# Kernel optimization log

Hardware: AMD Instinct MI355X
Metric: run time of the kernel (lower is better)

Reference implementation:

```python
import jax, jax.numpy as jnp
import numpy as np


def group_norm(x, gamma, beta, groups, eps=1e-5):
    B, C, H, W = x.shape
    xg = x.reshape(B, groups, C // groups, H, W)
    mu = xg.mean(axis=(2, 3, 4), keepdims=True)
    var = xg.var(axis=(2, 3, 4), keepdims=True)
    xn = ((xg - mu) * jax.lax.rsqrt(var + eps)).reshape(B, C, H, W)
    return xn * gamma[:, None, None] + beta[:, None, None]


def setup_inputs() -> dict:
    key = jax.random.key(0)
    ks = jax.random.split(key, 8)
    B, C, H, W = 4, 32, 256, 256
    return {
        "dec4": jax.random.normal(ks[0], (B, 512, 16, 16), jnp.float32),
        "feat": jax.random.normal(ks[1], (B, 64, H, W), jnp.float32),
        "gn_pre_gamma": jnp.ones((64,), jnp.float32),
        "gn_pre_beta": jnp.zeros((64,), jnp.float32),
        "W_pre": jax.random.normal(ks[2], (8, 64), jnp.float32) * 0.05,
        "b_pre": jnp.zeros((8,), jnp.float32),
        "gn_gap_gamma": jnp.ones((512,), jnp.float32),
        "gn_gap_beta": jnp.zeros((512,), jnp.float32),
        "W_gap": jax.random.normal(ks[3], (256, 512), jnp.float32) * 0.05,
        "b_gap": jnp.zeros((256,), jnp.float32),
        "emb": jax.random.normal(ks[4], (C, 256), jnp.float32),
        "W_ctrl": jax.random.normal(ks[5], (153, 512), jnp.float32) * 0.05,
        "b_ctrl": jnp.zeros((153,), jnp.float32),
    }


def reference(dec4, feat, gn_pre_gamma, gn_pre_beta, W_pre, b_pre,
              gn_gap_gamma, gn_gap_beta, W_gap, b_gap, emb, W_ctrl, b_ctrl):
    B = feat.shape[0]
    C = emb.shape[0]  # number of classes / dynamic-head instances
    # precls_conv: GroupNorm(16,64) -> ReLU -> 1x1 conv 64->8
    pre = jax.nn.relu(group_norm(feat, gn_pre_gamma, gn_pre_beta, 16))
    head_in = jnp.einsum('oi,bihw->bohw', W_pre, pre) + b_pre[:, None, None]  # [B,8,H,W]
    # GAP branch: GroupNorm(16,512) -> ReLU -> global avg pool -> 1x1 conv 512->256
    g = jax.nn.relu(group_norm(dec4, gn_gap_gamma, gn_gap_beta, 16)).mean(axis=(2, 3))  # [B,512]
    x_feat = g @ W_gap.T + b_gap  # [B,256]
    # controller: per (batch, class) dynamic conv params (1x1 conv == linear)
    x_cond = jnp.concatenate([
        jnp.broadcast_to(x_feat[:, None, :], (B, C, 256)),
        jnp.broadcast_to(emb[None], (B, C, 256)),
    ], axis=-1)  # [B,C,512]
    params = x_cond @ W_ctrl.T + b_ctrl  # [B,C,153]
    # split per weight_nums=[64,64,8], bias_nums=[8,8,1]
    w1 = params[..., 0:64].reshape(B, C, 8, 8)    # [out=8, in=8]
    w2 = params[..., 64:128].reshape(B, C, 8, 8)
    w3 = params[..., 128:136]                     # [out=1, in=8]
    b1 = params[..., 136:144]
    b2 = params[..., 144:152]
    b3 = params[..., 152:153]
    # batched grouped 1x1 convs (one group per (batch,class) instance)
    x1 = jax.nn.relu(jnp.einsum('bcoi,bihw->bcohw', w1, head_in) + b1[..., None, None])
    x2 = jax.nn.relu(jnp.einsum('bcoi,bcihw->bcohw', w2, x1) + b2[..., None, None])
    logits = jnp.einsum('bci,bcihw->bchw', w3, x2) + b3[..., None]  # [B,C,H,W]
    return logits
```

## Files before the change

kernel.cpp:

```cpp
#include <hip/hip_runtime.h>
#include <hip/hip_fp16.h>

typedef __fp16 h2 __attribute__((ext_vector_type(2)));
typedef __fp16 v4h __attribute__((ext_vector_type(4)));
typedef float f32x4 __attribute__((ext_vector_type(4)));

__device__ inline float wave_sum(float v) {
#pragma unroll
    for (int off = 32; off > 0; off >>= 1) v += __shfl_down(v, off, 64);
    return v;
}

__device__ inline v4h relu_pack(f32x4 d) {
    h2 lo = __builtin_amdgcn_cvt_pkrtz(d[0], d[1]);
    h2 hi = __builtin_amdgcn_cvt_pkrtz(d[2], d[3]);
#if defined(__has_builtin)
#if __has_builtin(__builtin_elementwise_max)
    h2 z = {(__fp16)0, (__fp16)0};
    lo = __builtin_elementwise_max(lo, z);
    hi = __builtin_elementwise_max(hi, z);
#else
    lo.x = (__fp16)fmaxf((float)lo.x, 0.f); lo.y = (__fp16)fmaxf((float)lo.y, 0.f);
    hi.x = (__fp16)fmaxf((float)hi.x, 0.f); hi.y = (__fp16)fmaxf((float)hi.y, 0.f);
#endif
#endif
    v4h r = {lo.x, lo.y, hi.x, hi.y};
    return r;
}

__global__ __launch_bounds__(256) void prep(
    const float* __restrict__ feat, const float* __restrict__ dec4,
    const float* __restrict__ gn_gap_gamma, const float* __restrict__ gn_gap_beta,
    const float* __restrict__ emb, const float* __restrict__ W_ctrl,
    float* __restrict__ partials, float* __restrict__ g_buf,
    float* __restrict__ E_ws) {
    int blk = blockIdx.x;
    int tid = threadIdx.x;
    int wid = tid >> 6, lane = tid & 63;
    if (blk < 512) {
        int grp = blk >> 3;
        int chunk = blk & 7;
        const float4* base = (const float4*)(feat + (size_t)grp * 262144 + (size_t)chunk * 32768);
        float sa = 0.f, qa = 0.f, sb = 0.f, qb = 0.f;
#pragma unroll 8
        for (int i = 0; i < 16; ++i) {
            float4 v = base[i * 256 + tid];
            float4 u = base[(i + 16) * 256 + tid];
            sa += v.x + v.y + v.z + v.w;
            qa += v.x * v.x + v.y * v.y + v.z * v.z + v.w * v.w;
            sb += u.x + u.y + u.z + u.w;
            qb += u.x * u.x + u.y * u.y + u.z * u.z + u.w * u.w;
        }
        __shared__ float ls[4], lq[4];
        float s = wave_sum(sa + sb);
        float q = wave_sum(qa + qb);
        if (lane == 0) { ls[wid] = s; lq[wid] = q; }
        __syncthreads();
        if (tid == 0) {
            partials[blk * 2 + 0] = ls[0] + ls[1] + ls[2] + ls[3];
            partials[blk * 2 + 1] = lq[0] + lq[1] + lq[2] + lq[3];
        }
    } else if (blk < 576) {
        int idx = blk - 512;
        int b = idx >> 4, gi = idx & 15;
        const float* base = dec4 + (size_t)idx * 8192;
        int ch = tid >> 3, sub = tid & 7;
        const float4* r = (const float4*)(base + ch * 256 + sub * 32);
        float v[32];
        float s = 0.f, q = 0.f;
#pragma unroll
        for (int i = 0; i < 8; ++i) {
            float4 a = r[i];
            v[i * 4 + 0] = a.x; v[i * 4 + 1] = a.y; v[i * 4 + 2] = a.z; v[i * 4 + 3] = a.w;
            s += a.x + a.y + a.z + a.w;
            q += a.x * a.x + a.y * a.y + a.z * a.z + a.w * a.w;
        }
        __shared__ float ls[4], lq[4], bc[2];
        s = wave_sum(s); q = wave_sum(q);
        if (lane == 0) { ls[wid] = s; lq[wid] = q; }
        __syncthreads();
        if (tid == 0) {
            float S = ls[0] + ls[1] + ls[2] + ls[3];
            float Q = lq[0] + lq[1] + lq[2] + lq[3];
            const float inv = 1.f / 8192.f;
            float mu = S * inv;
            float var = Q * inv - mu * mu;
            bc[0] = mu;
            bc[1] = rsqrtf(var + 1e-5f);
        }
        __syncthreads();
        float mu = bc[0], rs = bc[1];
        int c = gi * 32 + ch;
        float sc = rs * gn_gap_gamma[c];
        float sh = gn_gap_beta[c] - mu * sc;
        float acc = 0.f;
#pragma unroll
        for (int i = 0; i < 32; ++i) acc += fmaxf(v[i] * sc + sh, 0.f);
#pragma unroll
        for (int m = 1; m < 8; m <<= 1) acc += __shfl_xor(acc, m, 64);
        if (sub == 0) g_buf[b * 512 + c] = acc * (1.f / 256.f);
    } else {
        int c = blk - 576;
        __shared__ float es[256];
        es[tid] = emb[c * 256 + tid];
        __syncthreads();
        if (tid < 153) {
            const float4* w4 = (const float4*)(W_ctrl + tid * 512 + 256);
            const float4* e4 = (const float4*)es;
            float acc = 0.f;
#pragma unroll 8
            for (int k = 0; k < 64; ++k) {
                float4 a = w4[k], e = e4[k];
                acc += a.x * e.x + a.y * e.y + a.z * e.z + a.w * e.w;
            }
            E_ws[c * 153 + tid] = acc;
        }
    }
}

__global__ __launch_bounds__(256) void fc(
    const float* __restrict__ g_buf, const float* __restrict__ W_gap,
    const float* __restrict__ b_gap, const float* __restrict__ W_ctrl,
    const float* __restrict__ b_ctrl, const float* __restrict__ E_ws,
    unsigned char* __restrict__ pk) {
    int b = blockIdx.x, tid = threadIdx.x;
    __shared__ float gs[512];
    __shared__ float xf[256];
    __shared__ float F[160];
    gs[tid] = g_buf[b * 512 + tid];
    gs[tid + 256] = g_buf[b * 512 + 256 + tid];
    __syncthreads();
    {
        const float4* w = (const float4*)(W_gap + tid * 512);
        const float4* g4 = (const float4*)gs;
        float acc = b_gap[tid];
#pragma unroll 8
        for (int k = 0; k < 128; ++k) {
            float4 wv = w[k], gv = g4[k];
            acc += wv.x * gv.x + wv.y * gv.y + wv.z * gv.z + wv.w * gv.w;
        }
        xf[tid] = acc;
    }
    __syncthreads();
    if (tid < 160) {
        float acc = 0.f;
        if (tid < 153) {
            const float4* w = (const float4*)(W_ctrl + tid * 512);
            const float4* x4 = (const float4*)xf;
#pragma unroll 8
            for (int k = 0; k < 64; ++k) {
                float4 wv = w[k], xv = x4[k];
                acc += wv.x * xv.x + wv.y * xv.y + wv.z * xv.z + wv.w * xv.w;
            }
            acc += b_ctrl[tid];
        }
        F[tid] = acc;
    }
    __syncthreads();
    unsigned char* dst = pk + (size_t)b * 10240;
    for (int c = 0; c < 32; ++c) {
        if (tid < 152) {
            float v = F[tid] + E_ws[c * 153 + tid];
            ((__fp16*)(dst + c * 320))[tid] = (__fp16)v;
        } else if (tid == 152) {
            *(float*)(dst + c * 320 + 304) = F[152] + E_ws[c * 153 + 152];
        }
    }
}

struct Frags { v4h A1, A2, A3; f32x4 C1, C2, C3; };

__device__ inline Frags make_frags(const __fp16* ph, const float* smemf, int c0,
                                   int csel, int o, int dup, int crow,
                                   bool ok1, bool okBD) {
    Frags f;
    int cbA = (c0 + csel) * 160;
    int cbB = (c0 + crow) * 160;
    v4h z = {(__fp16)0, (__fp16)0, (__fp16)0, (__fp16)0};
    v4h a1 = *(const v4h*)(ph + cbA + o * 8 + dup * 4);
    v4h a2 = *(const v4h*)(ph + cbA + 64 + o * 8 + dup * 4);
    v4h a3 = *(const v4h*)(ph + cbA + 128 + dup * 4);
    f.A1 = ok1 ? a1 : z;
    f.A2 = okBD ? a2 : z;
    f.A3 = (okBD && o == 0) ? a3 : z;
    v4h b1 = *(const v4h*)(ph + cbB + 136 + dup * 4);
    v4h b2 = *(const v4h*)(ph + cbB + 144 + dup * 4);
    f.C1 = f32x4{(float)b1.x, (float)b1.y, (float)b1.z, (float)b1.w};
    f.C2 = f32x4{(float)b2.x, (float)b2.y, (float)b2.z, (float)b2.w};
    f.C3 = f32x4{0.f, 0.f, 0.f, 0.f};
    if (dup == 0) f.C3[0] = smemf[(c0 + crow) * 80 + 76];
    return f;
}

__global__ __launch_bounds__(512, 4) void mainK(
    const float* __restrict__ feat, const float* __restrict__ partials,
    const float* __restrict__ gamma, const float* __restrict__ beta,
    const float* __restrict__ W_pre, const float* __restrict__ b_pre,
    const float4* __restrict__ pk, float* __restrict__ out) {
    int blk = blockIdx.x;
    int b = blk >> 7;
    int tid = threadIdx.x;
    int w = tid >> 6, lane = tid & 63;
    int P0 = (blk & 127) << 9;

    __shared__ __align__(16) float smem[4768];
    float4* pp   = (float4*)smem;
    float4* hi_l = (float4*)(smem + 2560);
    float2* sch  = (float2*)(smem + 4608);
    float* mus = smem + 4736;
    float* rss = smem + 4752;

    const float4* src = pk + (size_t)b * 640;
    for (int i = tid; i < 640; i += 512) pp[i] = src[i];

    if (tid < 16) {
        float s = 0.f, q = 0.f;
#pragma unroll
        for (int cc = 0; cc < 8; ++cc) {
            int idx = ((b * 16 + tid) * 8 + cc) * 2;
            s += partials[idx]; q += partials[idx + 1];
        }
        const float inv = 1.f / 262144.f;
        float mu = s * inv;
        float var = q * inv - mu * mu;
        mus[tid] = mu; rss[tid] = rsqrtf(var + 1e-5f);
    }
    __syncthreads();
    if (tid < 64) {
        float mu = mus[tid >> 2], rs = rss[tid >> 2];
        float sg = rs * gamma[tid];
        sch[tid] = make_float2(sg, beta[tid] - mu * sg);
    }
    __syncthreads();

    {
        float hi[8];
#pragma unroll
        for (int o2 = 0; o2 < 8; ++o2) hi[o2] = b_pre[o2];
        const float* fb = feat + ((size_t)b << 22) + P0 + tid;
#pragma unroll
        for (int ch = 0; ch < 64; ++ch) {
            float v = fb[(size_t)ch << 16];
            float2 ss = sch[ch];
            float pre = fmaxf(v * ss.x + ss.y, 0.f);
#pragma unroll
            for (int o2 = 0; o2 < 8; ++o2) hi[o2] += W_pre[o2 * 64 + ch] * pre;
        }
        float4 hq;
        hq.x = __builtin_bit_cast(float, __builtin_amdgcn_cvt_pkrtz(hi[0], hi[1]));
        hq.y = __builtin_bit_cast(float, __builtin_amdgcn_cvt_pkrtz(hi[2], hi[3]));
        hq.z = __builtin_bit_cast(float, __builtin_amdgcn_cvt_pkrtz(hi[4], hi[5]));
        hq.w = __builtin_bit_cast(float, __builtin_amdgcn_cvt_pkrtz(hi[6], hi[7]));
        hi_l[tid] = hq;
    }
    __syncthreads();

    const __fp16* ph = (const __fp16*)smem;
    int m = lane & 15;
    int kg = lane >> 4;
    int csel = m >> 3;
    int o = m & 7;
    int dup = kg & 1;
    int crow = kg >> 1;
    bool ok1 = (kg < 2);
    bool okBD = (crow == csel);
    bool act = (dup == 0);

    int cA = w << 2;
    int cB = cA + 2;
    Frags fa = make_frags(ph, smem, cA, csel, o, dup, crow, ok1, okBD);
    Frags fb2 = make_frags(ph, smem, cB, csel, o, dup, crow, ok1, okBD);

    float* ob = out + ((size_t)b << 21) + P0;
    float* cpA = ob + ((size_t)(cA + crow) << 16) + m;
    float* cpB = ob + ((size_t)(cB + crow) << 16) + m;
    const __fp16* hp = ph + 5120 + m * 8 + dup * 4;

#pragma unroll 4
    for (int g = 0; g < 32; ++g) {
        v4h B1 = *(const v4h*)(hp + g * 128);
        f32x4 d1a = __builtin_amdgcn_mfma_f32_16x16x16f16(fa.A1, B1, fa.C1, 0, 0, 0);
        f32x4 d1b = __builtin_amdgcn_mfma_f32_16x16x16f16(fb2.A1, B1, fb2.C1, 0, 0, 0);
        v4h p2a = relu_pack(d1a);
        v4h p2b = relu_pack(d1b);
        f32x4 d2a = __builtin_amdgcn_mfma_f32_16x16x16f16(fa.A2, p2a, fa.C2, 0, 0, 0);
        f32x4 d2b = __builtin_amdgcn_mfma_f32_16x16x16f16(fb2.A2, p2b, fb2.C2, 0, 0, 0);
        v4h p3a = relu_pack(d2a);
        v4h p3b = relu_pack(d2b);
        f32x4 d3a = __builtin_amdgcn_mfma_f32_16x16x16f16(fa.A3, p3a, fa.C3, 0, 0, 0);
        f32x4 d3b = __builtin_amdgcn_mfma_f32_16x16x16f16(fb2.A3, p3b, fb2.C3, 0, 0, 0);
        if (act) {
            cpA[g * 16] = d3a[0];
            cpB[g * 16] = d3b[0];
        }
    }
}

extern "C" void kernel_launch(void* const* d_in, const int* in_sizes, int n_in,
                              void* d_out, int out_size, void* d_ws, size_t ws_size,
                              hipStream_t stream) {
    const float* dec4         = (const float*)d_in[0];
    const float* feat         = (const float*)d_in[1];
    const float* gn_pre_gamma = (const float*)d_in[2];
    const float* gn_pre_beta  = (const float*)d_in[3];
    const float* W_pre        = (const float*)d_in[4];
    const float* b_pre        = (const float*)d_in[5];
    const float* gn_gap_gamma = (const float*)d_in[6];
    const float* gn_gap_beta  = (const float*)d_in[7];
    const float* W_gap        = (const float*)d_in[8];
    const float* b_gap        = (const float*)d_in[9];
    const float* emb          = (const float*)d_in[10];
    const float* W_ctrl       = (const float*)d_in[11];
    const float* b_ctrl       = (const float*)d_in[12];
    float* out = (float*)d_out;
    float* ws  = (float*)d_ws;

    float* partials = ws;
    float* g_buf    = ws + 1024;
    float* E_ws     = ws + 3072;
    unsigned char* pkB = (unsigned char*)(ws + 7968);

    prep<<<608, 256, 0, stream>>>(feat, dec4, gn_gap_gamma, gn_gap_beta,
                                  emb, W_ctrl, partials, g_buf, E_ws);
    fc<<<4, 256, 0, stream>>>(g_buf, W_gap, b_gap, W_ctrl, b_ctrl, E_ws, pkB);
    mainK<<<512, 512, 0, stream>>>(feat, partials, gn_pre_gamma, gn_pre_beta,
                                   W_pre, b_pre, (const float4*)pkB, out);
}
```

Before: 73.32 us.

## Double grid size for stats and main kernels, split channel reduction across halves

The feature statistics pass now uses 16 chunks per group instead of 8, so it launches twice as many blocks, each doing half the work. The main kernel now processes 256 pixels per block instead of 512 and launches twice as many blocks. Within each block the two halves of the threads each reduce 32 of the 64 input channels, then combine their partial sums through shared memory. This is meant to raise parallelism and memory-level concurrency, at the cost of an extra shared-memory pass and barrier, more LDS per block, and a second reload of the per-batch parameter tile by each block.

```diff
diff --git a/kernel.cpp b/kernel.cpp
--- a/kernel.cpp
+++ b/kernel.cpp
@@ -14,16 +14,9 @@
 __device__ inline v4h relu_pack(f32x4 d) {
     h2 lo = __builtin_amdgcn_cvt_pkrtz(d[0], d[1]);
     h2 hi = __builtin_amdgcn_cvt_pkrtz(d[2], d[3]);
-#if defined(__has_builtin)
-#if __has_builtin(__builtin_elementwise_max)
     h2 z = {(__fp16)0, (__fp16)0};
     lo = __builtin_elementwise_max(lo, z);
     hi = __builtin_elementwise_max(hi, z);
-#else
-    lo.x = (__fp16)fmaxf((float)lo.x, 0.f); lo.y = (__fp16)fmaxf((float)lo.y, 0.f);
-    hi.x = (__fp16)fmaxf((float)hi.x, 0.f); hi.y = (__fp16)fmaxf((float)hi.y, 0.f);
-#endif
-#endif
     v4h r = {lo.x, lo.y, hi.x, hi.y};
     return r;
 }
@@ -37,15 +30,15 @@
     int blk = blockIdx.x;
     int tid = threadIdx.x;
     int wid = tid >> 6, lane = tid & 63;
-    if (blk < 512) {
-        int grp = blk >> 3;
-        int chunk = blk & 7;
-        const float4* base = (const float4*)(feat + (size_t)grp * 262144 + (size_t)chunk * 32768);
+    if (blk < 1024) {
+        int grp = blk >> 4;
+        int chunk = blk & 15;
+        const float4* base = (const float4*)(feat + (size_t)grp * 262144 + (size_t)chunk * 16384);
         float sa = 0.f, qa = 0.f, sb = 0.f, qb = 0.f;
-#pragma unroll 8
-        for (int i = 0; i < 16; ++i) {
+#pragma unroll 4
+        for (int i = 0; i < 8; ++i) {
             float4 v = base[i * 256 + tid];
-            float4 u = base[(i + 16) * 256 + tid];
+            float4 u = base[(i + 8) * 256 + tid];
             sa += v.x + v.y + v.z + v.w;
             qa += v.x * v.x + v.y * v.y + v.z * v.z + v.w * v.w;
             sb += u.x + u.y + u.z + u.w;
@@ -60,8 +53,8 @@
             partials[blk * 2 + 0] = ls[0] + ls[1] + ls[2] + ls[3];
             partials[blk * 2 + 1] = lq[0] + lq[1] + lq[2] + lq[3];
         }
-    } else if (blk < 576) {
-        int idx = blk - 512;
+    } else if (blk < 1088) {
+        int idx = blk - 1024;
         int b = idx >> 4, gi = idx & 15;
         const float* base = dec4 + (size_t)idx * 8192;
         int ch = tid >> 3, sub = tid & 7;
@@ -100,7 +93,7 @@
         for (int m = 1; m < 8; m <<= 1) acc += __shfl_xor(acc, m, 64);
         if (sub == 0) g_buf[b * 512 + c] = acc * (1.f / 256.f);
     } else {
-        int c = blk - 576;
+        int c = blk - 1088;
         __shared__ float es[256];
         es[tid] = emb[c * 256 + tid];
         __syncthreads();
@@ -198,17 +191,19 @@
     const float* __restrict__ W_pre, const float* __restrict__ b_pre,
     const float4* __restrict__ pk, float* __restrict__ out) {
     int blk = blockIdx.x;
-    int b = blk >> 7;
+    int b = blk >> 8;
     int tid = threadIdx.x;
     int w = tid >> 6, lane = tid & 63;
-    int P0 = (blk & 127) << 9;
-
-    __shared__ __align__(16) float smem[4768];
+    int P0 = (blk & 255) << 8;
+
+    __shared__ __align__(16) float smem[6816];
     float4* pp   = (float4*)smem;
-    float4* hi_l = (float4*)(smem + 2560);
-    float2* sch  = (float2*)(smem + 4608);
-    float* mus = smem + 4736;
-    float* rss = smem + 4752;
+    float4* tmpA = (float4*)(smem + 2560);
+    float4* tmpB = (float4*)(smem + 4608);
+    float4* hi_l = tmpA;
+    float2* sch  = (float2*)(smem + 6656);
+    float* mus = smem + 6784;
+    float* rss = smem + 6800;
 
     const float4* src = pk + (size_t)b * 640;
     for (int i = tid; i < 640; i += 512) pp[i] = src[i];
@@ -216,8 +211,8 @@
     if (tid < 16) {
         float s = 0.f, q = 0.f;
 #pragma unroll
-        for (int cc = 0; cc < 8; ++cc) {
-            int idx = ((b * 16 + tid) * 8 + cc) * 2;
+        for (int cc = 0; cc < 16; ++cc) {
+            int idx = ((b * 16 + tid) * 16 + cc) * 2;
             s += partials[idx]; q += partials[idx + 1];
         }
         const float inv = 1.f / 262144.f;
@@ -234,23 +229,33 @@
     __syncthreads();
 
     {
+        int px = tid & 255, half = tid >> 8;
         float hi[8];
 #pragma unroll
-        for (int o2 = 0; o2 < 8; ++o2) hi[o2] = b_pre[o2];
-        const float* fb = feat + ((size_t)b << 22) + P0 + tid;
-#pragma unroll
-        for (int ch = 0; ch < 64; ++ch) {
-            float v = fb[(size_t)ch << 16];
+        for (int o2 = 0; o2 < 8; ++o2) hi[o2] = half ? 0.f : b_pre[o2];
+        const float* fb = feat + ((size_t)b << 22) + ((size_t)half << 21) + P0 + px;
+        const float* wp = W_pre + half * 32;
+#pragma unroll
+        for (int c2 = 0; c2 < 32; ++c2) {
+            int ch = half * 32 + c2;
+            float v = fb[(size_t)c2 << 16];
             float2 ss = sch[ch];
             float pre = fmaxf(v * ss.x + ss.y, 0.f);
 #pragma unroll
-            for (int o2 = 0; o2 < 8; ++o2) hi[o2] += W_pre[o2 * 64 + ch] * pre;
-        }
+            for (int o2 = 0; o2 < 8; ++o2) hi[o2] += wp[o2 * 64 + c2] * pre;
+        }
+        tmpA[tid] = make_float4(hi[0], hi[1], hi[2], hi[3]);
+        tmpB[tid] = make_float4(hi[4], hi[5], hi[6], hi[7]);
+    }
+    __syncthreads();
+    if (tid < 256) {
+        float4 a0 = tmpA[tid], a1 = tmpA[tid + 256];
+        float4 b0 = tmpB[tid], b1 = tmpB[tid + 256];
         float4 hq;
-        hq.x = __builtin_bit_cast(float, __builtin_amdgcn_cvt_pkrtz(hi[0], hi[1]));
-        hq.y = __builtin_bit_cast(float, __builtin_amdgcn_cvt_pkrtz(hi[2], hi[3]));
-        hq.z = __builtin_bit_cast(float, __builtin_amdgcn_cvt_pkrtz(hi[4], hi[5]));
-        hq.w = __builtin_bit_cast(float, __builtin_amdgcn_cvt_pkrtz(hi[6], hi[7]));
+        hq.x = __builtin_bit_cast(float, __builtin_amdgcn_cvt_pkrtz(a0.x + a1.x, a0.y + a1.y));
+        hq.y = __builtin_bit_cast(float, __builtin_amdgcn_cvt_pkrtz(a0.z + a1.z, a0.w + a1.w));
+        hq.z = __builtin_bit_cast(float, __builtin_amdgcn_cvt_pkrtz(b0.x + b1.x, b0.y + b1.y));
+        hq.w = __builtin_bit_cast(float, __builtin_amdgcn_cvt_pkrtz(b0.z + b1.z, b0.w + b1.w));
         hi_l[tid] = hq;
     }
     __syncthreads();
@@ -277,7 +282,7 @@
     const __fp16* hp = ph + 5120 + m * 8 + dup * 4;
 
 #pragma unroll 4
-    for (int g = 0; g < 32; ++g) {
+    for (int g = 0; g < 16; ++g) {
         v4h B1 = *(const v4h*)(hp + g * 128);
         f32x4 d1a = __builtin_amdgcn_mfma_f32_16x16x16f16(fa.A1, B1, fa.C1, 0, 0, 0);
         f32x4 d1b = __builtin_amdgcn_mfma_f32_16x16x16f16(fb2.A1, B1, fb2.C1, 0, 0, 0);
@@ -316,13 +321,13 @@
     float* ws  = (float*)d_ws;
 
     float* partials = ws;
-    float* g_buf    = ws + 1024;
-    float* E_ws     = ws + 3072;
-    unsigned char* pkB = (unsigned char*)(ws + 7968);
-
-    prep<<<608, 256, 0, stream>>>(feat, dec4, gn_gap_gamma, gn_gap_beta,
-                                  emb, W_ctrl, partials, g_buf, E_ws);
+    float* g_buf    = ws + 2048;
+    float* E_ws     = ws + 4096;
+    unsigned char* pkB = (unsigned char*)(ws + 8992);
+
+    prep<<<1120, 256, 0, stream>>>(feat, dec4, gn_gap_gamma, gn_gap_beta,
+                                   emb, W_ctrl, partials, g_buf, E_ws);
     fc<<<4, 256, 0, stream>>>(g_buf, W_gap, b_gap, W_ctrl, b_ctrl, E_ws, pkB);
-    mainK<<<512, 512, 0, stream>>>(feat, partials, gn_pre_gamma, gn_pre_beta,
-                                   W_pre, b_pre, (const float4*)pkB, out);
-}
+    mainK<<<1024, 512, 0, stream>>>(feat, partials, gn_pre_gamma, gn_pre_beta,
+                                    W_pre, b_pre, (const float4*)pkB, out);
+}
```

New measurement: 88.06 us. 1.2x slower.

## Split main kernel into smaller 256-thread blocks over 128 pixels

Applied to the files above, without the earlier changes.

Each main-kernel block now covers 128 pixels with 256 threads (2048 blocks instead of 512), which shrinks shared memory and raises the occupancy target. Only 128 threads compute the head input, and each wave loops over four class pairs with one fragment set at a time instead of keeping two interleaved. The aim is more resident blocks to hide memory latency. The cost is redoing the per-batch setup (parameter copy, GroupNorm stats) four times as often, leaving half the threads idle during the feature pass, and losing the two independent MFMA chains per iteration.

```diff
diff --git a/kernel.cpp b/kernel.cpp
--- a/kernel.cpp
+++ b/kernel.cpp
@@ -14,16 +14,9 @@
 __device__ inline v4h relu_pack(f32x4 d) {
     h2 lo = __builtin_amdgcn_cvt_pkrtz(d[0], d[1]);
     h2 hi = __builtin_amdgcn_cvt_pkrtz(d[2], d[3]);
-#if defined(__has_builtin)
-#if __has_builtin(__builtin_elementwise_max)
     h2 z = {(__fp16)0, (__fp16)0};
     lo = __builtin_elementwise_max(lo, z);
     hi = __builtin_elementwise_max(hi, z);
-#else
-    lo.x = (__fp16)fmaxf((float)lo.x, 0.f); lo.y = (__fp16)fmaxf((float)lo.y, 0.f);
-    hi.x = (__fp16)fmaxf((float)hi.x, 0.f); hi.y = (__fp16)fmaxf((float)hi.y, 0.f);
-#endif
-#endif
     v4h r = {lo.x, lo.y, hi.x, hi.y};
     return r;
 }
@@ -192,26 +185,26 @@
     return f;
 }
 
-__global__ __launch_bounds__(512, 4) void mainK(
+__global__ __launch_bounds__(256, 8) void mainK(
     const float* __restrict__ feat, const float* __restrict__ partials,
     const float* __restrict__ gamma, const float* __restrict__ beta,
     const float* __restrict__ W_pre, const float* __restrict__ b_pre,
     const float4* __restrict__ pk, float* __restrict__ out) {
     int blk = blockIdx.x;
-    int b = blk >> 7;
+    int b = blk >> 9;
     int tid = threadIdx.x;
     int w = tid >> 6, lane = tid & 63;
-    int P0 = (blk & 127) << 9;
-
-    __shared__ __align__(16) float smem[4768];
+    int P0 = (blk & 511) << 7;
+
+    __shared__ __align__(16) float smem[3264];
     float4* pp   = (float4*)smem;
     float4* hi_l = (float4*)(smem + 2560);
-    float2* sch  = (float2*)(smem + 4608);
-    float* mus = smem + 4736;
-    float* rss = smem + 4752;
+    float2* sch  = (float2*)(smem + 3072);
+    float* mus = smem + 3200;
+    float* rss = smem + 3216;
 
     const float4* src = pk + (size_t)b * 640;
-    for (int i = tid; i < 640; i += 512) pp[i] = src[i];
+    for (int i = tid; i < 640; i += 256) pp[i] = src[i];
 
     if (tid < 16) {
         float s = 0.f, q = 0.f;
@@ -233,7 +226,7 @@
     }
     __syncthreads();
 
-    {
+    if (tid < 128) {
         float hi[8];
 #pragma unroll
         for (int o2 = 0; o2 < 8; ++o2) hi[o2] = b_pre[o2];
@@ -266,32 +259,23 @@
     bool okBD = (crow == csel);
     bool act = (dup == 0);
 
-    int cA = w << 2;
-    int cB = cA + 2;
-    Frags fa = make_frags(ph, smem, cA, csel, o, dup, crow, ok1, okBD);
-    Frags fb2 = make_frags(ph, smem, cB, csel, o, dup, crow, ok1, okBD);
-
     float* ob = out + ((size_t)b << 21) + P0;
-    float* cpA = ob + ((size_t)(cA + crow) << 16) + m;
-    float* cpB = ob + ((size_t)(cB + crow) << 16) + m;
     const __fp16* hp = ph + 5120 + m * 8 + dup * 4;
 
-#pragma unroll 4
-    for (int g = 0; g < 32; ++g) {
-        v4h B1 = *(const v4h*)(hp + g * 128);
-        f32x4 d1a = __builtin_amdgcn_mfma_f32_16x16x16f16(fa.A1, B1, fa.C1, 0, 0, 0);
-        f32x4 d1b = __builtin_amdgcn_mfma_f32_16x16x16f16(fb2.A1, B1, fb2.C1, 0, 0, 0);
-        v4h p2a = relu_pack(d1a);
-        v4h p2b = relu_pack(d1b);
-        f32x4 d2a = __builtin_amdgcn_mfma_f32_16x16x16f16(fa.A2, p2a, fa.C2, 0, 0, 0);
-        f32x4 d2b = __builtin_amdgcn_mfma_f32_16x16x16f16(fb2.A2, p2b, fb2.C2, 0, 0, 0);
-        v4h p3a = relu_pack(d2a);
-        v4h p3b = relu_pack(d2b);
-        f32x4 d3a = __builtin_amdgcn_mfma_f32_16x16x16f16(fa.A3, p3a, fa.C3, 0, 0, 0);
-        f32x4 d3b = __builtin_amdgcn_mfma_f32_16x16x16f16(fb2.A3, p3b, fb2.C3, 0, 0, 0);
-        if (act) {
-            cpA[g * 16] = d3a[0];
-            cpB[g * 16] = d3b[0];
+#pragma unroll 1
+    for (int p = 0; p < 4; ++p) {
+        int c0 = (w << 3) + (p << 1);
+        Frags f = make_frags(ph, smem, c0, csel, o, dup, crow, ok1, okBD);
+        float* cp = ob + ((size_t)(c0 + crow) << 16) + m;
+#pragma unroll 2
+        for (int g = 0; g < 8; ++g) {
+            v4h B1 = *(const v4h*)(hp + g * 128);
+            f32x4 d1 = __builtin_amdgcn_mfma_f32_16x16x16f16(f.A1, B1, f.C1, 0, 0, 0);
+            v4h p2 = relu_pack(d1);
+            f32x4 d2 = __builtin_amdgcn_mfma_f32_16x16x16f16(f.A2, p2, f.C2, 0, 0, 0);
+            v4h p3 = relu_pack(d2);
+            f32x4 d3 = __builtin_amdgcn_mfma_f32_16x16x16f16(f.A3, p3, f.C3, 0, 0, 0);
+            if (act) cp[g * 16] = d3[0];
         }
     }
 }
@@ -323,6 +307,6 @@
     prep<<<608, 256, 0, stream>>>(feat, dec4, gn_gap_gamma, gn_gap_beta,
                                   emb, W_ctrl, partials, g_buf, E_ws);
     fc<<<4, 256, 0, stream>>>(g_buf, W_gap, b_gap, W_ctrl, b_ctrl, E_ws, pkB);
-    mainK<<<512, 512, 0, stream>>>(feat, partials, gn_pre_gamma, gn_pre_beta,
-                                   W_pre, b_pre, (const float4*)pkB, out);
-}
+    mainK<<<2048, 256, 0, stream>>>(feat, partials, gn_pre_gamma, gn_pre_beta,
+                                    W_pre, b_pre, (const float4*)pkB, out);
+}
```

Result: slower. 79.65 us (+8.6%).

## Fuse prep, fc and main stages into one cooperative kernel with grid syncs

Applied to the files above, without the earlier changes.

Replaces the three-kernel launch sequence with a single cooperative kernel of 256 blocks of 512 threads. The stages are separated by grid.sync(), which removes two kernel-launch boundaries and their gaps. Each block now covers 1024 pixels instead of 512, and the fc stage splits its dot products across thread pairs. The fallback path still uses the old three kernels. In exchange, only 256 blocks run, with no occupancy hint, so there is less parallelism in the main phase, and the grid barriers add their own cost.

```diff
diff --git a/kernel.cpp b/kernel.cpp
--- a/kernel.cpp
+++ b/kernel.cpp
@@ -1,5 +1,8 @@
 #include <hip/hip_runtime.h>
 #include <hip/hip_fp16.h>
+#include <hip/hip_cooperative_groups.h>
+
+namespace cg = cooperative_groups;
 
 typedef __fp16 h2 __attribute__((ext_vector_type(2)));
 typedef __fp16 v4h __attribute__((ext_vector_type(4)));
@@ -14,158 +17,11 @@
 __device__ inline v4h relu_pack(f32x4 d) {
     h2 lo = __builtin_amdgcn_cvt_pkrtz(d[0], d[1]);
     h2 hi = __builtin_amdgcn_cvt_pkrtz(d[2], d[3]);
-#if defined(__has_builtin)
-#if __has_builtin(__builtin_elementwise_max)
     h2 z = {(__fp16)0, (__fp16)0};
     lo = __builtin_elementwise_max(lo, z);
     hi = __builtin_elementwise_max(hi, z);
-#else
-    lo.x = (__fp16)fmaxf((float)lo.x, 0.f); lo.y = (__fp16)fmaxf((float)lo.y, 0.f);
-    hi.x = (__fp16)fmaxf((float)hi.x, 0.f); hi.y = (__fp16)fmaxf((float)hi.y, 0.f);
-#endif
-#endif
     v4h r = {lo.x, lo.y, hi.x, hi.y};
     return r;
-}
-
-__global__ __launch_bounds__(256) void prep(
-    const float* __restrict__ feat, const float* __restrict__ dec4,
-    const float* __restrict__ gn_gap_gamma, const float* __restrict__ gn_gap_beta,
-    const float* __restrict__ emb, const float* __restrict__ W_ctrl,
-    float* __restrict__ partials, float* __restrict__ g_buf,
-    float* __restrict__ E_ws) {
-    int blk = blockIdx.x;
-    int tid = threadIdx.x;
-    int wid = tid >> 6, lane = tid & 63;
-    if (blk < 512) {
-        int grp = blk >> 3;
-        int chunk = blk & 7;
-        const float4* base = (const float4*)(feat + (size_t)grp * 262144 + (size_t)chunk * 32768);
-        float sa = 0.f, qa = 0.f, sb = 0.f, qb = 0.f;
-#pragma unroll 8
-        for (int i = 0; i < 16; ++i) {
-            float4 v = base[i * 256 + tid];
-            float4 u = base[(i + 16) * 256 + tid];
-            sa += v.x + v.y + v.z + v.w;
-            qa += v.x * v.x + v.y * v.y + v.z * v.z + v.w * v.w;
-            sb += u.x + u.y + u.z + u.w;
-            qb += u.x * u.x + u.y * u.y + u.z * u.z + u.w * u.w;
-        }
-        __shared__ float ls[4], lq[4];
-        float s = wave_sum(sa + sb);
-        float q = wave_sum(qa + qb);
-        if (lane == 0) { ls[wid] = s; lq[wid] = q; }
-        __syncthreads();
-        if (tid == 0) {
-            partials[blk * 2 + 0] = ls[0] + ls[1] + ls[2] + ls[3];
-            partials[blk * 2 + 1] = lq[0] + lq[1] + lq[2] + lq[3];
-        }
-    } else if (blk < 576) {
-        int idx = blk - 512;
-        int b = idx >> 4, gi = idx & 15;
-        const float* base = dec4 + (size_t)idx * 8192;
-        int ch = tid >> 3, sub = tid & 7;
-        const float4* r = (const float4*)(base + ch * 256 + sub * 32);
-        float v[32];
-        float s = 0.f, q = 0.f;
-#pragma unroll
-        for (int i = 0; i < 8; ++i) {
-            float4 a = r[i];
-            v[i * 4 + 0] = a.x; v[i * 4 + 1] = a.y; v[i * 4 + 2] = a.z; v[i * 4 + 3] = a.w;
-            s += a.x + a.y + a.z + a.w;
-            q += a.x * a.x + a.y * a.y + a.z * a.z + a.w * a.w;
-        }
-        __shared__ float ls[4], lq[4], bc[2];
-        s = wave_sum(s); q = wave_sum(q);
-        if (lane == 0) { ls[wid] = s; lq[wid] = q; }
-        __syncthreads();
-        if (tid == 0) {
-            float S = ls[0] + ls[1] + ls[2] + ls[3];
-            float Q = lq[0] + lq[1] + lq[2] + lq[3];
-            const float inv = 1.f / 8192.f;
-            float mu = S * inv;
-            float var = Q * inv - mu * mu;
-            bc[0] = mu;
-            bc[1] = rsqrtf(var + 1e-5f);
-        }
-        __syncthreads();
-        float mu = bc[0], rs = bc[1];
-        int c = gi * 32 + ch;
-        float sc = rs * gn_gap_gamma[c];
-        float sh = gn_gap_beta[c] - mu * sc;
-        float acc = 0.f;
-#pragma unroll
-        for (int i = 0; i < 32; ++i) acc += fmaxf(v[i] * sc + sh, 0.f);
-#pragma unroll
-        for (int m = 1; m < 8; m <<= 1) acc += __shfl_xor(acc, m, 64);
-        if (sub == 0) g_buf[b * 512 + c] = acc * (1.f / 256.f);
-    } else {
-        int c = blk - 576;
-        __shared__ float es[256];
-        es[tid] = emb[c * 256 + tid];
-        __syncthreads();
-        if (tid < 153) {
-            const float4* w4 = (const float4*)(W_ctrl + tid * 512 + 256);
-            const float4* e4 = (const float4*)es;
-            float acc = 0.f;
-#pragma unroll 8
-            for (int k = 0; k < 64; ++k) {
-                float4 a = w4[k], e = e4[k];
-                acc += a.x * e.x + a.y * e.y + a.z * e.z + a.w * e.w;
-            }
-            E_ws[c * 153 + tid] = acc;
-        }
-    }
-}
-
-__global__ __launch_bounds__(256) void fc(
-    const float* __restrict__ g_buf, const float* __restrict__ W_gap,
-    const float* __restrict__ b_gap, const float* __restrict__ W_ctrl,
-    const float* __restrict__ b_ctrl, const float* __restrict__ E_ws,
-    unsigned char* __restrict__ pk) {
-    int b = blockIdx.x, tid = threadIdx.x;
-    __shared__ float gs[512];
-    __shared__ float xf[256];
-    __shared__ float F[160];
-    gs[tid] = g_buf[b * 512 + tid];
-    gs[tid + 256] = g_buf[b * 512 + 256 + tid];
-    __syncthreads();
-    {
-        const float4* w = (const float4*)(W_gap + tid * 512);
-        const float4* g4 = (const float4*)gs;
-        float acc = b_gap[tid];
-#pragma unroll 8
-        for (int k = 0; k < 128; ++k) {
-            float4 wv = w[k], gv = g4[k];
-            acc += wv.x * gv.x + wv.y * gv.y + wv.z * gv.z + wv.w * gv.w;
-        }
-        xf[tid] = acc;
-    }
-    __syncthreads();
-    if (tid < 160) {
-        float acc = 0.f;
-        if (tid < 153) {
-            const float4* w = (const float4*)(W_ctrl + tid * 512);
-            const float4* x4 = (const float4*)xf;
-#pragma unroll 8
-            for (int k = 0; k < 64; ++k) {
-                float4 wv = w[k], xv = x4[k];
-                acc += wv.x * xv.x + wv.y * xv.y + wv.z * xv.z + wv.w * xv.w;
-            }
-            acc += b_ctrl[tid];
-        }
-        F[tid] = acc;
-    }
-    __syncthreads();
-    unsigned char* dst = pk + (size_t)b * 10240;
-    for (int c = 0; c < 32; ++c) {
-        if (tid < 152) {
-            float v = F[tid] + E_ws[c * 153 + tid];
-            ((__fp16*)(dst + c * 320))[tid] = (__fp16)v;
-        } else if (tid == 152) {
-            *(float*)(dst + c * 320 + 304) = F[152] + E_ws[c * 153 + 152];
-        }
-    }
 }
 
 struct Frags { v4h A1, A2, A3; f32x4 C1, C2, C3; };
@@ -192,6 +48,396 @@
     return f;
 }
 
+__global__ __launch_bounds__(512) void mega(
+    const float* __restrict__ feat, const float* __restrict__ dec4,
+    const float* __restrict__ gn_pre_gamma, const float* __restrict__ gn_pre_beta,
+    const float* __restrict__ W_pre, const float* __restrict__ b_pre,
+    const float* __restrict__ gn_gap_gamma, const float* __restrict__ gn_gap_beta,
+    const float* __restrict__ W_gap, const float* __restrict__ b_gap,
+    const float* __restrict__ emb, const float* __restrict__ W_ctrl,
+    const float* __restrict__ b_ctrl, float* __restrict__ out,
+    float* __restrict__ partials, float* __restrict__ g_buf,
+    float* __restrict__ E_ws, unsigned char* __restrict__ pk) {
+    cg::grid_group grid = cg::this_grid();
+    __shared__ __align__(16) float smem[6816];
+    const int k = blockIdx.x;
+    const int tid = threadIdx.x;
+    const int w = tid >> 6, lane = tid & 63;
+    float* ls = smem + 6656;
+    float* lq = smem + 6664;
+    float* bc = smem + 6672;
+
+    for (int t = k; t < 608; t += 256) {
+        if (t < 512) {
+            int grp = t >> 3, chunk = t & 7;
+            const float4* base = (const float4*)(feat + (size_t)grp * 262144 + (size_t)chunk * 32768);
+            float sa = 0.f, qa = 0.f, sb = 0.f, qb = 0.f;
+#pragma unroll 4
+            for (int i = 0; i < 8; ++i) {
+                float4 v = base[i * 512 + tid];
+                float4 u = base[(i + 8) * 512 + tid];
+                sa += v.x + v.y + v.z + v.w;
+                qa += v.x * v.x + v.y * v.y + v.z * v.z + v.w * v.w;
+                sb += u.x + u.y + u.z + u.w;
+                qb += u.x * u.x + u.y * u.y + u.z * u.z + u.w * u.w;
+            }
+            float s = wave_sum(sa + sb);
+            float q = wave_sum(qa + qb);
+            if (lane == 0) { ls[w] = s; lq[w] = q; }
+            __syncthreads();
+            if (tid == 0) {
+                float S = 0.f, Q = 0.f;
+#pragma unroll
+                for (int i = 0; i < 8; ++i) { S += ls[i]; Q += lq[i]; }
+                partials[t * 2 + 0] = S;
+                partials[t * 2 + 1] = Q;
+            }
+        } else if (t < 576) {
+            int idx = t - 512;
+            int b = idx >> 4, gi = idx & 15;
+            const float* base = dec4 + (size_t)idx * 8192;
+            int ch = tid >> 4, sub = tid & 15;
+            const float4* r = (const float4*)(base + ch * 256 + sub * 16);
+            float v[16];
+            float s = 0.f, q = 0.f;
+#pragma unroll
+            for (int i = 0; i < 4; ++i) {
+                float4 a = r[i];
+                v[i * 4 + 0] = a.x; v[i * 4 + 1] = a.y; v[i * 4 + 2] = a.z; v[i * 4 + 3] = a.w;
+                s += a.x + a.y + a.z + a.w;
+                q += a.x * a.x + a.y * a.y + a.z * a.z + a.w * a.w;
+            }
+            s = wave_sum(s); q = wave_sum(q);
+            if (lane == 0) { ls[w] = s; lq[w] = q; }
+            __syncthreads();
+            if (tid == 0) {
+                float S = 0.f, Q = 0.f;
+#pragma unroll
+                for (int i = 0; i < 8; ++i) { S += ls[i]; Q += lq[i]; }
+                const float inv = 1.f / 8192.f;
+                float mu = S * inv;
+                float var = Q * inv - mu * mu;
+                bc[0] = mu;
+                bc[1] = rsqrtf(var + 1e-5f);
+            }
+            __syncthreads();
+            float mu = bc[0], rs = bc[1];
+            int c = gi * 32 + ch;
+            float sc = rs * gn_gap_gamma[c];
+            float sh = gn_gap_beta[c] - mu * sc;
+            float acc = 0.f;
+#pragma unroll
+            for (int i = 0; i < 16; ++i) acc += fmaxf(v[i] * sc + sh, 0.f);
+#pragma unroll
+            for (int m = 1; m < 16; m <<= 1) acc += __shfl_xor(acc, m, 64);
+            if (sub == 0) g_buf[b * 512 + c] = acc * (1.f / 256.f);
+        } else {
+            int c = t - 576;
+            if (tid < 256) smem[tid] = emb[c * 256 + tid];
+            __syncthreads();
+            if (tid < 153) {
+                const float4* w4 = (const float4*)(W_ctrl + tid * 512 + 256);
+                const float4* e4 = (const float4*)smem;
+                float acc = 0.f;
+#pragma unroll 8
+                for (int kk = 0; kk < 64; ++kk) {
+                    float4 a = w4[kk], e = e4[kk];
+                    acc += a.x * e.x + a.y * e.y + a.z * e.z + a.w * e.w;
+                }
+                E_ws[c * 153 + tid] = acc;
+            }
+        }
+        __syncthreads();
+    }
+
+    grid.sync();
+
+    if (k < 4) {
+        int b = k;
+        float* gs = smem;
+        float* xf = smem + 512;
+        float* F  = smem + 768;
+        gs[tid] = g_buf[b * 512 + tid];
+        __syncthreads();
+        {
+            int o = tid >> 1, h = tid & 1;
+            const float4* wrow = (const float4*)(W_gap + o * 512 + h * 256);
+            const float4* gg = (const float4*)(gs + h * 256);
+            float acc = 0.f;
+#pragma unroll 8
+            for (int kk = 0; kk < 64; ++kk) {
+                float4 a = wrow[kk], g = gg[kk];
+                acc += a.x * g.x + a.y * g.y + a.z * g.z + a.w * g.w;
+            }
+            acc += __shfl_xor(acc, 1, 64);
+            if (h == 0) xf[o] = acc + b_gap[o];
+        }
+        __syncthreads();
+        if (tid < 306) {
+            int o = tid >> 1, h = tid & 1;
+            const float4* wrow = (const float4*)(W_ctrl + o * 512 + h * 128);
+            const float4* xx = (const float4*)(xf + h * 128);
+            float acc = 0.f;
+#pragma unroll 8
+            for (int kk = 0; kk < 32; ++kk) {
+                float4 a = wrow[kk], x = xx[kk];
+                acc += a.x * x.x + a.y * x.y + a.z * x.z + a.w * x.w;
+            }
+            acc += __shfl_xor(acc, 1, 64);
+            if (h == 0) F[o] = acc + b_ctrl[o];
+        }
+        __syncthreads();
+        unsigned char* dst = pk + (size_t)b * 10240;
+        for (int i = tid; i < 5120; i += 512) {
+            int c = i / 160, oo = i - c * 160;
+            if (oo < 152) {
+                ((__fp16*)(dst + c * 320))[oo] = (__fp16)(F[oo] + E_ws[c * 153 + oo]);
+            } else if (oo == 152) {
+                *(float*)(dst + c * 320 + 304) = F[152] + E_ws[c * 153 + 152];
+            }
+        }
+    }
+
+    grid.sync();
+
+    {
+        int b = k >> 6;
+        int P0 = (k & 63) << 10;
+        float4* pp   = (float4*)smem;
+        float4* hi_l = (float4*)(smem + 2560);
+        float2* sch  = (float2*)(smem + 6656);
+        float* mus = smem + 6784;
+        float* rss = smem + 6800;
+
+        const float4* src = (const float4*)(pk + (size_t)b * 10240);
+        for (int i = tid; i < 640; i += 512) pp[i] = src[i];
+
+        if (tid < 16) {
+            float s = 0.f, q = 0.f;
+#pragma unroll
+            for (int cc = 0; cc < 8; ++cc) {
+                int idx = ((b * 16 + tid) * 8 + cc) * 2;
+                s += partials[idx]; q += partials[idx + 1];
+            }
+            const float inv = 1.f / 262144.f;
+            float mu = s * inv;
+            float var = q * inv - mu * mu;
+            mus[tid] = mu; rss[tid] = rsqrtf(var + 1e-5f);
+        }
+        __syncthreads();
+        if (tid < 64) {
+            float mu = mus[tid >> 2], rs = rss[tid >> 2];
+            float sg = rs * gn_pre_gamma[tid];
+            sch[tid] = make_float2(sg, gn_pre_beta[tid] - mu * sg);
+        }
+        __syncthreads();
+
+#pragma unroll 1
+        for (int hh = 0; hh < 2; ++hh) {
+            int px = (hh << 9) + tid;
+            float hi[8];
+#pragma unroll
+            for (int o2 = 0; o2 < 8; ++o2) hi[o2] = b_pre[o2];
+            const float* fb = feat + ((size_t)b << 22) + P0 + px;
+#pragma unroll
+            for (int ch = 0; ch < 64; ++ch) {
+                float v = fb[(size_t)ch << 16];
+                float2 ss = sch[ch];
+                float pre = fmaxf(v * ss.x + ss.y, 0.f);
+#pragma unroll
+                for (int o2 = 0; o2 < 8; ++o2) hi[o2] += W_pre[o2 * 64 + ch] * pre;
+            }
+            float4 hq;
+            hq.x = __builtin_bit_cast(float, __builtin_amdgcn_cvt_pkrtz(hi[0], hi[1]));
+            hq.y = __builtin_bit_cast(float, __builtin_amdgcn_cvt_pkrtz(hi[2], hi[3]));
+            hq.z = __builtin_bit_cast(float, __builtin_amdgcn_cvt_pkrtz(hi[4], hi[5]));
+            hq.w = __builtin_bit_cast(float, __builtin_amdgcn_cvt_pkrtz(hi[6], hi[7]));
+            hi_l[px] = hq;
+        }
+        __syncthreads();
+
+        const __fp16* ph = (const __fp16*)smem;
+        int m = lane & 15;
+        int kg = lane >> 4;
+        int csel = m >> 3;
+        int o = m & 7;
+        int dup = kg & 1;
+        int crow = kg >> 1;
+        bool ok1 = (kg < 2);
+        bool okBD = (crow == csel);
+        bool act = (dup == 0);
+
+        int cA = w << 2;
+        int cB = cA + 2;
+        Frags fa = make_frags(ph, smem, cA, csel, o, dup, crow, ok1, okBD);
+        Frags fb2 = make_frags(ph, smem, cB, csel, o, dup, crow, ok1, okBD);
+
+        float* ob = out + ((size_t)b << 21) + P0;
+        float* cpA = ob + ((size_t)(cA + crow) << 16) + m;
+        float* cpB = ob + ((size_t)(cB + crow) << 16) + m;
+        const __fp16* hp = ph + 5120 + m * 8 + dup * 4;
+
+#pragma unroll 4
+        for (int g = 0; g < 64; ++g) {
+            v4h B1 = *(const v4h*)(hp + g * 128);
+            f32x4 d1a = __builtin_amdgcn_mfma_f32_16x16x16f16(fa.A1, B1, fa.C1, 0, 0, 0);
+            f32x4 d1b = __builtin_amdgcn_mfma_f32_16x16x16f16(fb2.A1, B1, fb2.C1, 0, 0, 0);
+            v4h p2a = relu_pack(d1a);
+            v4h p2b = relu_pack(d1b);
+            f32x4 d2a = __builtin_amdgcn_mfma_f32_16x16x16f16(fa.A2, p2a, fa.C2, 0, 0, 0);
+            f32x4 d2b = __builtin_amdgcn_mfma_f32_16x16x16f16(fb2.A2, p2b, fb2.C2, 0, 0, 0);
+            v4h p3a = relu_pack(d2a);
+            v4h p3b = relu_pack(d2b);
+            f32x4 d3a = __builtin_amdgcn_mfma_f32_16x16x16f16(fa.A3, p3a, fa.C3, 0, 0, 0);
+            f32x4 d3b = __builtin_amdgcn_mfma_f32_16x16x16f16(fb2.A3, p3b, fb2.C3, 0, 0, 0);
+            if (act) {
+                cpA[g * 16] = d3a[0];
+                cpB[g * 16] = d3b[0];
+            }
+        }
+    }
+}
+
+__global__ __launch_bounds__(256) void prep(
+    const float* __restrict__ feat, const float* __restrict__ dec4,
+    const float* __restrict__ gn_gap_gamma, const float* __restrict__ gn_gap_beta,
+    const float* __restrict__ emb, const float* __restrict__ W_ctrl,
+    float* __restrict__ partials, float* __restrict__ g_buf,
+    float* __restrict__ E_ws) {
+    int blk = blockIdx.x;
+    int tid = threadIdx.x;
+    int wid = tid >> 6, lane = tid & 63;
+    if (blk < 512) {
+        int grp = blk >> 3;
+        int chunk = blk & 7;
+        const float4* base = (const float4*)(feat + (size_t)grp * 262144 + (size_t)chunk * 32768);
+        float sa = 0.f, qa = 0.f, sb = 0.f, qb = 0.f;
+#pragma unroll 8
+        for (int i = 0; i < 16; ++i) {
+            float4 v = base[i * 256 + tid];
+            float4 u = base[(i + 16) * 256 + tid];
+            sa += v.x + v.y + v.z + v.w;
+            qa += v.x * v.x + v.y * v.y + v.z * v.z + v.w * v.w;
+            sb += u.x + u.y + u.z + u.w;
+            qb += u.x * u.x + u.y * u.y + u.z * u.z + u.w * u.w;
+        }
+        __shared__ float ls[4], lq[4];
+        float s = wave_sum(sa + sb);
+        float q = wave_sum(qa + qb);
+        if (lane == 0) { ls[wid] = s; lq[wid] = q; }
+        __syncthreads();
+        if (tid == 0) {
+            partials[blk * 2 + 0] = ls[0] + ls[1] + ls[2] + ls[3];
+            partials[blk * 2 + 1] = lq[0] + lq[1] + lq[2] + lq[3];
+        }
+    } else if (blk < 576) {
+        int idx = blk - 512;
+        int b = idx >> 4, gi = idx & 15;
+        const float* base = dec4 + (size_t)idx * 8192;
+        int ch = tid >> 3, sub = tid & 7;
+        const float4* r = (const float4*)(base + ch * 256 + sub * 32);
+        float v[32];
+        float s = 0.f, q = 0.f;
+#pragma unroll
+        for (int i = 0; i < 8; ++i) {
+            float4 a = r[i];
+            v[i * 4 + 0] = a.x; v[i * 4 + 1] = a.y; v[i * 4 + 2] = a.z; v[i * 4 + 3] = a.w;
+            s += a.x + a.y + a.z + a.w;
+            q += a.x * a.x + a.y * a.y + a.z * a.z + a.w * a.w;
+        }
+        __shared__ float ls[4], lq[4], bc[2];
+        s = wave_sum(s); q = wave_sum(q);
+        if (lane == 0) { ls[wid] = s; lq[wid] = q; }
+        __syncthreads();
+        if (tid == 0) {
+            float S = ls[0] + ls[1] + ls[2] + ls[3];
+            float Q = lq[0] + lq[1] + lq[2] + lq[3];
+            const float inv = 1.f / 8192.f;
+            float mu = S * inv;
+            float var = Q * inv - mu * mu;
+            bc[0] = mu;
+            bc[1] = rsqrtf(var + 1e-5f);
+        }
+        __syncthreads();
+        float mu = bc[0], rs = bc[1];
+        int c = gi * 32 + ch;
+        float sc = rs * gn_gap_gamma[c];
+        float sh = gn_gap_beta[c] - mu * sc;
+        float acc = 0.f;
+#pragma unroll
+        for (int i = 0; i < 32; ++i) acc += fmaxf(v[i] * sc + sh, 0.f);
+#pragma unroll
+        for (int m = 1; m < 8; m <<= 1) acc += __shfl_xor(acc, m, 64);
+        if (sub == 0) g_buf[b * 512 + c] = acc * (1.f / 256.f);
+    } else {
+        int c = blk - 576;
+        __shared__ float es[256];
+        es[tid] = emb[c * 256 + tid];
+        __syncthreads();
+        if (tid < 153) {
+            const float4* w4 = (const float4*)(W_ctrl + tid * 512 + 256);
+            const float4* e4 = (const float4*)es;
+            float acc = 0.f;
+#pragma unroll 8
+            for (int kk = 0; kk < 64; ++kk) {
+                float4 a = w4[kk], e = e4[kk];
+                acc += a.x * e.x + a.y * e.y + a.z * e.z + a.w * e.w;
+            }
+            E_ws[c * 153 + tid] = acc;
+        }
+    }
+}
+
+__global__ __launch_bounds__(256) void fc(
+    const float* __restrict__ g_buf, const float* __restrict__ W_gap,
+    const float* __restrict__ b_gap, const float* __restrict__ W_ctrl,
+    const float* __restrict__ b_ctrl, const float* __restrict__ E_ws,
+    unsigned char* __restrict__ pk) {
+    int b = blockIdx.x, tid = threadIdx.x;
+    __shared__ float gs[512];
+    __shared__ float xf[256];
+    __shared__ float F[160];
+    gs[tid] = g_buf[b * 512 + tid];
+    gs[tid + 256] = g_buf[b * 512 + 256 + tid];
+    __syncthreads();
+    {
+        const float4* w = (const float4*)(W_gap + tid * 512);
+        const float4* g4 = (const float4*)gs;
+        float acc = b_gap[tid];
+#pragma unroll 8
+        for (int kk = 0; kk < 128; ++kk) {
+            float4 wv = w[kk], gv = g4[kk];
+            acc += wv.x * gv.x + wv.y * gv.y + wv.z * gv.z + wv.w * gv.w;
+        }
+        xf[tid] = acc;
+    }
+    __syncthreads();
+    if (tid < 160) {
+        float acc = 0.f;
+        if (tid < 153) {
+            const float4* w = (const float4*)(W_ctrl + tid * 512);
+            const float4* x4 = (const float4*)xf;
+#pragma unroll 8
+            for (int kk = 0; kk < 64; ++kk) {
+                float4 wv = w[kk], xv = x4[kk];
+                acc += wv.x * xv.x + wv.y * xv.y + wv.z * xv.z + wv.w * xv.w;
+            }
+            acc += b_ctrl[tid];
+        }
+        F[tid] = acc;
+    }
+    __syncthreads();
+    unsigned char* dst = pk + (size_t)b * 10240;
+    for (int c = 0; c < 32; ++c) {
+        if (tid < 152) {
+            float v = F[tid] + E_ws[c * 153 + tid];
+            ((__fp16*)(dst + c * 320))[tid] = (__fp16)v;
+        } else if (tid == 152) {
+            *(float*)(dst + c * 320 + 304) = F[152] + E_ws[c * 153 + 152];
+        }
+    }
+}
+
 __global__ __launch_bounds__(512, 4) void mainK(
     const float* __restrict__ feat, const float* __restrict__ partials,
     const float* __restrict__ gamma, const float* __restrict__ beta,
@@ -320,9 +566,19 @@
     float* E_ws     = ws + 3072;
     unsigned char* pkB = (unsigned char*)(ws + 7968);
 
-    prep<<<608, 256, 0, stream>>>(feat, dec4, gn_gap_gamma, gn_gap_beta,
-                                  emb, W_ctrl, partials, g_buf, E_ws);
-    fc<<<4, 256, 0, stream>>>(g_buf, W_gap, b_gap, W_ctrl, b_ctrl, E_ws, pkB);
-    mainK<<<512, 512, 0, stream>>>(feat, partials, gn_pre_gamma, gn_pre_beta,
-                                   W_pre, b_pre, (const float4*)pkB, out);
-}
+    void* args[] = {
+        (void*)&feat, (void*)&dec4, (void*)&gn_pre_gamma, (void*)&gn_pre_beta,
+        (void*)&W_pre, (void*)&b_pre, (void*)&gn_gap_gamma, (void*)&gn_gap_beta,
+        (void*)&W_gap, (void*)&b_gap, (void*)&emb, (void*)&W_ctrl, (void*)&b_ctrl,
+        (void*)&out, (void*)&partials, (void*)&g_buf, (void*)&E_ws, (void*)&pkB
+    };
+    hipError_t err = hipLaunchCooperativeKernel((void*)mega, dim3(256), dim3(512),
+                                                args, 0, stream);
+    if (err != hipSuccess) {
+        prep<<<608, 256, 0, stream>>>(feat, dec4, gn_gap_gamma, gn_gap_beta,
+                                      emb, W_ctrl, partials, g_buf, E_ws);
+        fc<<<4, 256, 0, stream>>>(g_buf, W_gap, b_gap, W_ctrl, b_ctrl, E_ws, pkB);
+        mainK<<<512, 512, 0, stream>>>(feat, partials, gn_pre_gamma, gn_pre_beta,
+                                       W_pre, b_pre, (const float4*)pkB, out);
+    }
+}
```

New measurement: 182.9 us. +149.4%, slower.
